# Optimization experiments

Measured on AMD Instinct MI355X. Metric: run time of the kernel, lower is better.

## Reference

```python
import jax, jax.numpy as jnp
import numpy as np

BETA = 0.25  # commitment loss weight


def setup_inputs() -> dict:
    key = jax.random.key(0)
    k1, k2 = jax.random.split(key)
    B, D, H, W = 16, 256, 64, 64
    K = 2048  # num_codebook
    z = jax.random.normal(k1, (B, D, H, W), dtype=jnp.float32)
    # matches nn.Embedding init uniform_(-1/K, 1/K) in scale-free way; values irrelevant to math
    codebook = jax.random.uniform(k2, (K, D), dtype=jnp.float32,
                                  minval=-1.0 / K, maxval=1.0 / K)
    return {"z": z, "codebook": codebook}


def reference(z, codebook):
    # z: (B, D, H, W) -> (B, H, W, D) -> (N, D)
    b, d, h, w = z.shape
    k = codebook.shape[0]
    z_flat = jnp.transpose(z, (0, 2, 3, 1)).reshape(-1, d)  # (N, D)

    # squared L2 distance via sum-of-squares + matmul (same expansion as torch code)
    distance = (jnp.sum(z_flat * z_flat, axis=1, keepdims=True)
                + jnp.sum(codebook * codebook, axis=1)
                - 2.0 * jnp.matmul(z_flat, codebook.T))  # (N, K)
    vq_indices = jnp.argmin(distance, axis=1)  # (N,)
    z_quantized = codebook[vq_indices]  # (N, D) gather

    # one-hot counting (scatter-add, equivalent to sum of one-hot)
    vq_current_count = jnp.zeros((k,), dtype=jnp.int32).at[vq_indices].add(1)

    sg = jax.lax.stop_gradient
    codebook_loss = jnp.mean((z_quantized - sg(z_flat)) ** 2)
    commitment_loss = jnp.mean((z_flat - sg(z_quantized)) ** 2)
    loss = codebook_loss + BETA * commitment_loss

    # straight-through estimator
    z_st = z_flat + sg(z_quantized - z_flat)
    q = jnp.transpose(z_st.reshape(b, h, w, d), (0, 3, 1, 2))  # (B, D, H, W)
    return q, loss, codebook_loss, commitment_loss, vq_current_count
```

## Files before the change

### kernel.cpp

```cpp
#include <hip/hip_runtime.h>

#define N_TOT 65536
#define K_CB  2048
#define D_DIM 256
#define HW    4096
#define DHW   1048576

typedef _Float16 half8 __attribute__((ext_vector_type(8)));
typedef _Float16 half4v __attribute__((ext_vector_type(4)));
typedef float f32x16 __attribute__((ext_vector_type(16)));


__device__ __forceinline__ void gload_lds16(const void* g, void* l) {
    __builtin_amdgcn_global_load_lds((const __attribute__((address_space(1))) void*)g,
                                     (__attribute__((address_space(3))) void*)l, 16, 0, 0);
}

__device__ __forceinline__ float pw128_sq(const float* __restrict__ base, int stride) {
    #pragma clang fp contract(off)
    float r[8];
    #pragma unroll
    for (int j = 0; j < 8; ++j) { float v = base[j * stride]; r[j] = v * v; }
    for (int i = 8; i < 128; i += 8) {
        #pragma unroll
        for (int j = 0; j < 8; ++j) { float v = base[(i + j) * stride]; r[j] += v * v; }
    }
    return ((r[0] + r[1]) + (r[2] + r[3])) + ((r[4] + r[5]) + (r[6] + r[7]));
}

__global__ void cbnorm_zero_kernel(const float* __restrict__ cb, float* __restrict__ cb2,
                                   int* __restrict__ counts, float* __restrict__ sse) {
    #pragma clang fp contract(off)
    int k = blockIdx.x * 256 + threadIdx.x;
    const float* row = cb + (size_t)k * D_DIM;
    cb2[k] = pw128_sq(row, 1) + pw128_sq(row + 128, 1);
    counts[k] = 0;
    if (k == 0) *sse = 0.f;
}

__global__ void split_c_kernel(const float* __restrict__ cb,
                               _Float16* __restrict__ ch, _Float16* __restrict__ cl) {
    int e = (blockIdx.x * 256 + threadIdx.x) * 4;
    float4 v = *(const float4*)(cb + e);
    float xs[4] = {v.x, v.y, v.z, v.w};
    half4v hh, hl;
    #pragma unroll
    for (int u = 0; u < 4; ++u) {
        float x = xs[u] * 16384.0f;
        _Float16 hv = (_Float16)x;
        hh[u] = hv;
        hl[u] = (_Float16)(x - (float)hv);
    }
    *(half4v*)(ch + e) = hh;
    *(half4v*)(cl + e) = hl;
}

__global__ void fused_z_kernel(const float* __restrict__ z,
                               _Float16* __restrict__ zh, _Float16* __restrict__ zl,
                               float* __restrict__ z2,
                               unsigned long long* __restrict__ rowmin_g) {
    __shared__ __align__(16) float lt[256 * 33];
    __shared__ float rj[512];
    __shared__ float hh[64];
    int t = threadIdx.x;
    int n0 = blockIdx.x * 32;
    int b = n0 >> 12, s0 = n0 & 4095;
    const float* zb = z + (size_t)b * DHW + s0;

    #pragma unroll
    for (int v = 0; v < 8; ++v) {
        int f = v * 256 + t;
        int d = f >> 3, nch = f & 7;
        float4 val = *(const float4*)(zb + (size_t)d * HW + nch * 4);
        lt[d * 33 + nch * 4 + 0] = val.x;
        lt[d * 33 + nch * 4 + 1] = val.y;
        lt[d * 33 + nch * 4 + 2] = val.z;
        lt[d * 33 + nch * 4 + 3] = val.w;
    }
    __syncthreads();

    {
        #pragma clang fp contract(off)
        int n = t & 31, j = t >> 5;
        #pragma unroll
        for (int hf = 0; hf < 2; ++hf) {
            float r = 0.f;
            #pragma unroll
            for (int i = 0; i < 16; ++i) {
                float v = lt[(hf * 128 + i * 8 + j) * 33 + n];
                r += v * v;
            }
            rj[n * 16 + hf * 8 + j] = r;
        }
    }

    #pragma unroll
    for (int v = 0; v < 8; ++v) {
        int g = v * 256 + t;
        int n = g >> 6, du = g & 63;
        half4v hv, lv;
        #pragma unroll
        for (int u = 0; u < 4; ++u) {
            float x = lt[(du * 4 + u) * 33 + n] * 2048.0f;
            _Float16 h = (_Float16)x;
            hv[u] = h;
            lv[u] = (_Float16)(x - (float)h);
        }
        size_t off = (size_t)(n0 + n) * 256 + du * 4;
        *(half4v*)(zh + off) = hv;
        *(half4v*)(zl + off) = lv;
    }
    __syncthreads();

    if (t < 64) {
        #pragma clang fp contract(off)
        int n = t & 31, hf = t >> 5;
        const float* r = &rj[n * 16 + hf * 8];
        hh[hf * 32 + n] = ((r[0] + r[1]) + (r[2] + r[3])) + ((r[4] + r[5]) + (r[6] + r[7]));
    }
    __syncthreads();
    if (t < 32) {
        #pragma clang fp contract(off)
        z2[n0 + t] = hh[t] + hh[32 + t];
        rowmin_g[n0 + t] = ~0ull;
    }
}


__device__ __forceinline__ void stage_tile(int ki,
        const _Float16* __restrict__ zh, const _Float16* __restrict__ zl,
        const _Float16* __restrict__ ch, const _Float16* __restrict__ cl,
        int r0, int c0, int t, _Float16* la, _Float16* lb) {
    int seg  = ki >> 2;
    int koff = (ki & 3) * 64;
    const _Float16* asrc = (seg < 2) ? zh : zl;
    const _Float16* bsrc = (seg == 1) ? cl : ch;
    #pragma unroll
    for (int v = 0; v < 4; ++v) {
        int p = v * 512 + t;
        int row = p >> 3;
        int ku = (p & 7) ^ (row & 7);
        gload_lds16(asrc + (size_t)(r0 + row) * 256 + koff + ku * 8, la + (size_t)p * 8);
    }
    #pragma unroll
    for (int v = 0; v < 4; ++v) {
        int p = v * 512 + t;
        int row = p >> 3;
        int ku = (p & 7) ^ (row & 7);
        gload_lds16(bsrc + (size_t)(c0 + row) * 256 + koff + ku * 8, lb + (size_t)p * 8);
    }
}

__device__ __forceinline__ void compute_tile(const _Float16* la, const _Float16* lb,
        int wm, int wn, int l31, int l5, f32x16 acc[4][2]) {
    #pragma unroll
    for (int ks = 0; ks < 4; ++ks) {
        half8 af[4], bf[2];
        #pragma unroll
        for (int i = 0; i < 4; ++i) {
            int row = wm * 128 + i * 32 + l31;
            int ku  = (ks * 2 + l5) ^ (row & 7);
            af[i] = *(const half8*)(la + row * 64 + ku * 8);
        }
        #pragma unroll
        for (int j = 0; j < 2; ++j) {
            int row = wn * 64 + j * 32 + l31;
            int ku  = (ks * 2 + l5) ^ (row & 7);
            bf[j] = *(const half8*)(lb + row * 64 + ku * 8);
        }
        #pragma unroll
        for (int i = 0; i < 4; ++i)
            #pragma unroll
            for (int j = 0; j < 2; ++j)
                acc[i][j] = __builtin_amdgcn_mfma_f32_32x32x16_f16(af[i], bf[j], acc[i][j], 0, 0, 0);
    }
}

__device__ __forceinline__ unsigned long long kmin_xor(unsigned long long key, int m) {
    unsigned lo = (unsigned)key, hi = (unsigned)(key >> 32);
    unsigned olo = __shfl_xor(lo, m);
    unsigned ohi = __shfl_xor(hi, m);
    unsigned long long o = ((unsigned long long)ohi << 32) | olo;
    return (o < key) ? o : key;
}

__launch_bounds__(512, 2)
__global__ void argmin_mfma_kernel(const _Float16* __restrict__ zh, const _Float16* __restrict__ zl,
                                   const _Float16* __restrict__ ch, const _Float16* __restrict__ cl,
                                   const float* __restrict__ cb2, const float* __restrict__ z2arr,
                                   unsigned long long* __restrict__ rowmin_g) {
    __shared__ __align__(16) char lds_raw[131072];
    _Float16* a0 = (_Float16*)lds_raw;
    _Float16* b0 = (_Float16*)(lds_raw + 32768);
    _Float16* a1 = (_Float16*)(lds_raw + 65536);
    _Float16* b1 = (_Float16*)(lds_raw + 98304);

    int t = threadIdx.x;
    int bid = blockIdx.x;
    int swz = (bid & 7) * 256 + (bid >> 3);
    int r0 = (swz >> 3) * 256;
    int c0 = (swz & 7) * 256;
    int w = t >> 6, lane = t & 63;
    int wm = w >> 2, wn = w & 3;
    int l31 = lane & 31, l5 = lane >> 5;

    f32x16 acc[4][2];
    #pragma unroll
    for (int i = 0; i < 4; ++i)
        #pragma unroll
        for (int j = 0; j < 2; ++j)
            #pragma unroll
            for (int r = 0; r < 16; ++r) acc[i][j][r] = 0.f;

    float c2v[2];
    #pragma unroll
    for (int j = 0; j < 2; ++j)
        c2v[j] = cb2[c0 + wn * 64 + j * 32 + l31];

    stage_tile(0, zh, zl, ch, cl, r0, c0, t, a0, b0);
    __syncthreads();

    #pragma unroll 1
    for (int kp = 0; kp < 6; ++kp) {
        stage_tile(kp * 2 + 1, zh, zl, ch, cl, r0, c0, t, a1, b1);
        compute_tile(a0, b0, wm, wn, l31, l5, acc);
        __syncthreads();
        if (kp < 5)
            stage_tile(kp * 2 + 2, zh, zl, ch, cl, r0, c0, t, a0, b0);
        compute_tile(a1, b1, wm, wn, l31, l5, acc);
        __syncthreads();
    }

    unsigned long long* scratch = (unsigned long long*)lds_raw;
    #pragma unroll
    for (int i = 0; i < 4; ++i) {
        #pragma unroll
        for (int rg = 0; rg < 16; ++rg) {
            int rowoff = (rg & 3) + 8 * (rg >> 2) + 4 * l5;
            int m = wm * 128 + i * 32 + rowoff;
            float zz = z2arr[r0 + m];
            unsigned long long key = ~0ull;
            #pragma unroll
            for (int j = 0; j < 2; ++j) {
                float sc = (zz + c2v[j]) - acc[i][j][rg] * (1.0f / 16777216.0f);
                unsigned long long k2 = ((unsigned long long)__float_as_uint(sc) << 32)
                                      | (unsigned)(c0 + wn * 64 + j * 32 + l31);
                key = (k2 < key) ? k2 : key;
            }
            key = kmin_xor(key, 16);
            key = kmin_xor(key, 8);
            if (l31 < 8) scratch[m * 34 + wn * 8 + l31] = key;
        }
    }
    __syncthreads();
    if (t < 256) {
        const ulonglong2* srow = (const ulonglong2*)(scratch + t * 34);
        unsigned long long best = ~0ull;
        #pragma unroll
        for (int s = 0; s < 16; ++s) {
            ulonglong2 p = srow[s];
            if (p.x < best) best = p.x;
            if (p.y < best) best = p.y;
        }
        atomicMin(&rowmin_g[r0 + t], best);
    }
}

__global__ void gather_kernel(const float* __restrict__ z, const float* __restrict__ cb,
                              const unsigned long long* __restrict__ rowmin_g,
                              float* __restrict__ qout,
                              float* __restrict__ sse, int* __restrict__ counts) {
    int t = threadIdx.x;
    int si = t & 63, dg = t >> 6;
    int n = blockIdx.x * 64 + si;
    int idx = (int)(rowmin_g[n] & 0xFFFFFFFFull);
    int b = n >> 12, s = n & 4095;
    const float* zb = z + (size_t)b * DHW + s;
    float*       qb = qout + (size_t)b * DHW + s;
    const float4* crow = (const float4*)(cb + (size_t)idx * D_DIM + dg * 64);
    float acc = 0.f;
    #pragma unroll
    for (int dd4 = 0; dd4 < 16; ++dd4) {
        float4 q4 = crow[dd4];
        float qv[4] = {q4.x, q4.y, q4.z, q4.w};
        #pragma unroll
        for (int u = 0; u < 4; ++u) {
            int d = dg * 64 + dd4 * 4 + u;
            float zv = zb[(size_t)d * HW];
            qb[(size_t)d * HW] = qv[u];
            float df = zv - qv[u];
            acc += df * df;
        }
    }
    #pragma unroll
    for (int off = 32; off > 0; off >>= 1) acc += __shfl_down(acc, off, 64);
    if ((t & 63) == 0) atomicAdd(sse, acc);
    if (dg == 0) atomicAdd(&counts[idx], 1);
}

__global__ void finalize_kernel(const float* __restrict__ sse, const int* __restrict__ counts,
                                float* __restrict__ out) {
    int t = threadIdx.x;
    float mse = *sse * (1.0f / 16777216.0f);
    if (t == 0) {
        out[16777216] = mse * 1.25f;
        out[16777217] = mse;
        out[16777218] = mse;
    }
    for (int i = t; i < 2048; i += 256) out[16777219 + i] = (float)counts[i];
}

extern "C" void kernel_launch(void* const* d_in, const int* in_sizes, int n_in,
                              void* d_out, int out_size, void* d_ws, size_t ws_size,
                              hipStream_t stream) {
    const float* z  = (const float*)d_in[0];
    const float* cb = (const float*)d_in[1];
    float* out = (float*)d_out;
    float* ws  = (float*)d_ws;

    float* cb2    = ws;
    int*   counts = (int*)(ws + 2048);
    float* sse    = ws + 4096;
    float* z2     = ws + 4352;
    unsigned long long* rowmin_g = (unsigned long long*)(ws + 69888);
    _Float16* ch  = (_Float16*)(ws + 200960);
    _Float16* cl  = (_Float16*)(ws + 463104);

    _Float16* zzh = (_Float16*)d_out;
    _Float16* zzl = zzh + 16777216;

    cbnorm_zero_kernel<<<8, 256, 0, stream>>>(cb, cb2, counts, sse);
    split_c_kernel<<<512, 256, 0, stream>>>(cb, ch, cl);
    fused_z_kernel<<<2048, 256, 0, stream>>>(z, zzh, zzl, z2, rowmin_g);
    argmin_mfma_kernel<<<2048, 512, 0, stream>>>(zzh, zzl, ch, cl, cb2, z2, rowmin_g);
    gather_kernel<<<1024, 256, 0, stream>>>(z, cb, rowmin_g, out, sse, counts);
    finalize_kernel<<<1, 256, 0, stream>>>(sse, counts, out);
}
```

Before: 488.5 us.

## Interleave global-to-LDS prefetch with MFMA sub-steps using explicit barriers and priority

Rewrites the GEMM main loop as a fine-grained schedule. Each K tile is split into four sub-steps, and the next tile's B and A global-to-LDS loads are issued inside the first two sub-steps instead of all at once. Each sub-step uses sched_barrier, s_barrier and s_setprio around the MFMA block so that memory issue and matrix math overlap across waves. The cost is more workgroup barriers per tile, and a manual vmcnt wait replaces the previous __syncthreads placement.

```diff
diff --git a/kernel.cpp b/kernel.cpp
--- a/kernel.cpp
+++ b/kernel.cpp
@@ -127,55 +127,6 @@
 }
 
 
-__device__ __forceinline__ void stage_tile(int ki,
-        const _Float16* __restrict__ zh, const _Float16* __restrict__ zl,
-        const _Float16* __restrict__ ch, const _Float16* __restrict__ cl,
-        int r0, int c0, int t, _Float16* la, _Float16* lb) {
-    int seg  = ki >> 2;
-    int koff = (ki & 3) * 64;
-    const _Float16* asrc = (seg < 2) ? zh : zl;
-    const _Float16* bsrc = (seg == 1) ? cl : ch;
-    #pragma unroll
-    for (int v = 0; v < 4; ++v) {
-        int p = v * 512 + t;
-        int row = p >> 3;
-        int ku = (p & 7) ^ (row & 7);
-        gload_lds16(asrc + (size_t)(r0 + row) * 256 + koff + ku * 8, la + (size_t)p * 8);
-    }
-    #pragma unroll
-    for (int v = 0; v < 4; ++v) {
-        int p = v * 512 + t;
-        int row = p >> 3;
-        int ku = (p & 7) ^ (row & 7);
-        gload_lds16(bsrc + (size_t)(c0 + row) * 256 + koff + ku * 8, lb + (size_t)p * 8);
-    }
-}
-
-__device__ __forceinline__ void compute_tile(const _Float16* la, const _Float16* lb,
-        int wm, int wn, int l31, int l5, f32x16 acc[4][2]) {
-    #pragma unroll
-    for (int ks = 0; ks < 4; ++ks) {
-        half8 af[4], bf[2];
-        #pragma unroll
-        for (int i = 0; i < 4; ++i) {
-            int row = wm * 128 + i * 32 + l31;
-            int ku  = (ks * 2 + l5) ^ (row & 7);
-            af[i] = *(const half8*)(la + row * 64 + ku * 8);
-        }
-        #pragma unroll
-        for (int j = 0; j < 2; ++j) {
-            int row = wn * 64 + j * 32 + l31;
-            int ku  = (ks * 2 + l5) ^ (row & 7);
-            bf[j] = *(const half8*)(lb + row * 64 + ku * 8);
-        }
-        #pragma unroll
-        for (int i = 0; i < 4; ++i)
-            #pragma unroll
-            for (int j = 0; j < 2; ++j)
-                acc[i][j] = __builtin_amdgcn_mfma_f32_32x32x16_f16(af[i], bf[j], acc[i][j], 0, 0, 0);
-    }
-}
-
 __device__ __forceinline__ unsigned long long kmin_xor(unsigned long long key, int m) {
     unsigned lo = (unsigned)key, hi = (unsigned)(key >> 32);
     unsigned olo = __shfl_xor(lo, m);
@@ -217,19 +168,76 @@
     for (int j = 0; j < 2; ++j)
         c2v[j] = cb2[c0 + wn * 64 + j * 32 + l31];
 
-    stage_tile(0, zh, zl, ch, cl, r0, c0, t, a0, b0);
+    auto stage_A = [&](int ki, _Float16* na) {
+        int seg = ki >> 2, koff = (ki & 3) * 64;
+        const _Float16* asrc = (seg < 2) ? zh : zl;
+        #pragma unroll
+        for (int v = 0; v < 4; ++v) {
+            int p = v * 512 + t;
+            int row = p >> 3;
+            int ku = (p & 7) ^ (row & 7);
+            gload_lds16(asrc + (size_t)(r0 + row) * 256 + koff + ku * 8, na + (size_t)p * 8);
+        }
+    };
+    auto stage_B = [&](int ki, _Float16* nb) {
+        int seg = ki >> 2, koff = (ki & 3) * 64;
+        const _Float16* bsrc = (seg == 1) ? cl : ch;
+        #pragma unroll
+        for (int v = 0; v < 4; ++v) {
+            int p = v * 512 + t;
+            int row = p >> 3;
+            int ku = (p & 7) ^ (row & 7);
+            gload_lds16(bsrc + (size_t)(c0 + row) * 256 + koff + ku * 8, nb + (size_t)p * 8);
+        }
+    };
+
+    auto tile4 = [&](const _Float16* la, const _Float16* lb, _Float16* na, _Float16* nb,
+                     int nki, bool ds) {
+        #pragma unroll
+        for (int ks = 0; ks < 4; ++ks) {
+            __builtin_amdgcn_sched_barrier(0);
+            half8 af[4], bf[2];
+            #pragma unroll
+            for (int i = 0; i < 4; ++i) {
+                int row = wm * 128 + i * 32 + l31;
+                int ku  = (ks * 2 + l5) ^ (row & 7);
+                af[i] = *(const half8*)(la + row * 64 + ku * 8);
+            }
+            #pragma unroll
+            for (int j = 0; j < 2; ++j) {
+                int row = wn * 64 + j * 32 + l31;
+                int ku  = (ks * 2 + l5) ^ (row & 7);
+                bf[j] = *(const half8*)(lb + row * 64 + ku * 8);
+            }
+            if (ds && ks == 0) stage_B(nki, nb);
+            if (ds && ks == 1) stage_A(nki, na);
+            __builtin_amdgcn_sched_barrier(0);
+            __builtin_amdgcn_s_barrier();
+            __builtin_amdgcn_s_setprio(1);
+            #pragma unroll
+            for (int i = 0; i < 4; ++i)
+                #pragma unroll
+                for (int j = 0; j < 2; ++j)
+                    acc[i][j] = __builtin_amdgcn_mfma_f32_32x32x16_f16(af[i], bf[j], acc[i][j], 0, 0, 0);
+            __builtin_amdgcn_s_setprio(0);
+            __builtin_amdgcn_sched_barrier(0);
+            if (ks == 3) {
+                asm volatile("s_waitcnt vmcnt(0)" ::: "memory");
+            }
+            __builtin_amdgcn_s_barrier();
+        }
+    };
+
+    stage_B(0, b0);
+    stage_A(0, a0);
     __syncthreads();
 
     #pragma unroll 1
     for (int kp = 0; kp < 6; ++kp) {
-        stage_tile(kp * 2 + 1, zh, zl, ch, cl, r0, c0, t, a1, b1);
-        compute_tile(a0, b0, wm, wn, l31, l5, acc);
-        __syncthreads();
-        if (kp < 5)
-            stage_tile(kp * 2 + 2, zh, zl, ch, cl, r0, c0, t, a0, b0);
-        compute_tile(a1, b1, wm, wn, l31, l5, acc);
-        __syncthreads();
-    }
+        tile4(a0, b0, a1, b1, 2 * kp + 1, true);
+        tile4(a1, b1, a0, b0, 2 * kp + 2, kp < 5);
+    }
+    __syncthreads();
 
     unsigned long long* scratch = (unsigned long long*)lds_raw;
     #pragma unroll
```

New measurement: 496.3 us. About the same (+1.6%).
